# Kernel optimization log

Hardware: AMD Instinct MI355X
Metric: run time of the kernel (lower is better)

The kernel has to match this reference:

```python
import jax, jax.numpy as jnp
import numpy as np

B, N, D_POINTS, D_MODEL = 2, 2048, 32, 512


def _gather(feat, idx):
    # feat: [B, N, C], idx: [B, N, K] -> [B, N, K, C]
    return jax.vmap(lambda f, i: f[i])(feat, idx)


def setup_inputs() -> dict:
    key = jax.random.key(0)
    ks = jax.random.split(key, 20)
    def lin(k, fan_in, fan_out):
        bound = 1.0 / np.sqrt(fan_in)
        return jax.random.uniform(k, (fan_in, fan_out), jnp.float32, -bound, bound)
    def bias(k, fan_in, fan_out):
        bound = 1.0 / np.sqrt(fan_in)
        return jax.random.uniform(k, (fan_out,), jnp.float32, -bound, bound)
    return {
        "xyz": jax.random.normal(ks[0], (B, N, 3), jnp.float32),
        "points": jax.random.normal(ks[1], (B, N, D_POINTS), jnp.float32),
        "fc1_w": lin(ks[2], D_POINTS, D_MODEL), "fc1_b": bias(ks[3], D_POINTS, D_MODEL),
        "fc2_w": lin(ks[4], D_MODEL, D_POINTS), "fc2_b": bias(ks[5], D_MODEL, D_POINTS),
        "delta_w1": lin(ks[6], 3, D_MODEL), "delta_b1": bias(ks[7], 3, D_MODEL),
        "delta_w2": lin(ks[8], D_MODEL, D_MODEL), "delta_b2": bias(ks[9], D_MODEL, D_MODEL),
        "gamma_w1": lin(ks[10], D_MODEL, D_MODEL), "gamma_b1": bias(ks[11], D_MODEL, D_MODEL),
        "gamma_w2": lin(ks[12], D_MODEL, D_MODEL), "gamma_b2": bias(ks[13], D_MODEL, D_MODEL),
        "wq": lin(ks[14], D_MODEL, D_MODEL),
        "wk": lin(ks[15], D_MODEL, D_MODEL),
        "wv": lin(ks[16], D_MODEL, D_MODEL),
        "knn_k": 16,
    }


def reference(xyz, points, fc1_w, fc1_b, fc2_w, fc2_b,
              delta_w1, delta_b1, delta_w2, delta_b2,
              gamma_w1, gamma_b1, gamma_w2, gamma_b2,
              wq, wk, wv, knn_k):
    # square_distance: [B, N, N]
    sq = jnp.sum(xyz * xyz, axis=-1)
    dists = sq[:, :, None] + sq[:, None, :] - 2.0 * jnp.einsum('bnc,bmc->bnm', xyz, xyz)
    # knn: k smallest distances (argsort[:, :, :k] equivalent)
    _, knn_idx = jax.lax.top_k(-dists, knn_k)           # [B, N, K]
    knn_xyz = _gather(xyz, knn_idx)                      # [B, N, K, 3]

    pre = points
    x = points @ fc1_w + fc1_b                           # [B, N, d_model]
    q = x @ wq                                           # [B, N, d_model]
    k = _gather(x @ wk, knn_idx)                         # [B, N, K, d_model]
    v = _gather(x @ wv, knn_idx)                         # [B, N, K, d_model]

    # positional encoding MLP on delta xyz
    delta = xyz[:, :, None, :] - knn_xyz                 # [B, N, K, 3]
    pos_enc = jax.nn.relu(delta @ delta_w1 + delta_b1) @ delta_w2 + delta_b2

    # gamma MLP on (q - k + pos_enc)
    a = q[:, :, None, :] - k + pos_enc
    a = jax.nn.relu(a @ gamma_w1 + gamma_b1) @ gamma_w2 + gamma_b2

    scale = jnp.asarray(np.sqrt(D_MODEL), a.dtype)
    attn = jax.nn.softmax(a / scale, axis=-2)            # softmax over neighbors, per channel

    res = jnp.sum(attn * (v + pos_enc), axis=2)          # einsum 'bmnf,bmnf->bmf'
    res = res @ fc2_w + fc2_b + pre                      # [B, N, d_points]
    return res, attn
```

## Files before the change

kernel.cpp:

```cpp
#include <hip/hip_runtime.h>
#include <hip/hip_bf16.h>
#include <math.h>

typedef __bf16 bf16_t;
typedef float f32x4 __attribute__((ext_vector_type(4)));
typedef bf16_t bf16x8 __attribute__((ext_vector_type(8)));

#define BM 128
#define BN 128
#define BKT 32
#define NT 16

#define GLD_LDS16(gp, lp) __builtin_amdgcn_global_load_lds( \
    (const __attribute__((address_space(1))) void*)(gp), \
    (__attribute__((address_space(3))) void*)(lp), 16, 0, 0)

struct TC7 { const float* src[7]; bf16_t* dst[7]; };
__global__ __launch_bounds__(256) void tcast7_kernel(TC7 tc) {
  int job = blockIdx.x >> 10;
  int idx = (blockIdx.x & 1023) * 256 + threadIdx.x;
  if (job < 4) {
    int n = idx >> 9, k = idx & 511;
    tc.dst[job][idx] = (bf16_t)tc.src[job][k * 512 + n];
  } else {
    tc.dst[job][idx] = (bf16_t)tc.src[job][idx];
  }
}

__global__ __launch_bounds__(256) void cc_kernel(const float* __restrict__ db2, const float* __restrict__ gw1,
                                                 const float* __restrict__ gb1, float* __restrict__ cc) {
  int n = blockIdx.x * 256 + threadIdx.x;
  float s = gb1[n];
  for (int d = 0; d < 512; ++d) s = fmaf(db2[d], gw1[d * 512 + n], s);
  cc[n] = s;
}

__global__ __launch_bounds__(256) void knn_kernel(const float* __restrict__ xyz, int* __restrict__ knn) {
  __shared__ float sx[2048], sy[2048], sz[2048], sq[2048];
  int tid = threadIdx.x;
  int lane = tid & 63, wave = tid >> 6;
  int gq = blockIdx.x * 4 + wave;
  int b  = gq >> 11;
  int base = b << 11;
  for (int p = tid; p < 2048; p += 256) {
    float x = xyz[(base + p) * 3 + 0];
    float y = xyz[(base + p) * 3 + 1];
    float z = xyz[(base + p) * 3 + 2];
    sx[p] = x; sy[p] = y; sz[p] = z;
    sq[p] = __fadd_rn(__fadd_rn(__fmul_rn(x, x), __fmul_rn(y, y)), __fmul_rn(z, z));
  }
  __syncthreads();
  int iq = gq & 2047;
  float qx = sx[iq], qy = sy[iq], qz = sz[iq], sqi = sq[iq];

  unsigned long long key[32];
  #pragma unroll
  for (int j = 0; j < 32; ++j) {
    int p = lane + j * 64;
    float d = __fmul_rn(sx[p], qx);
    d = fmaf(sy[p], qy, d);
    d = fmaf(sz[p], qz, d);
    float dist = __fsub_rn(__fadd_rn(sqi, sq[p]), __fmul_rn(2.0f, d));
    unsigned int bits = __float_as_uint(dist);
    unsigned int sk = bits ^ (unsigned int)(((int)bits >> 31) | 0x80000000);
    key[j] = ((unsigned long long)sk << 32) | (unsigned int)p;
  }

  int r = 0;
  #pragma unroll 1
  for (int s = 0; s < 16; ++s) {
    unsigned long long m = key[0];
    #pragma unroll
    for (int j = 1; j < 32; ++j) m = (key[j] < m) ? key[j] : m;
    #pragma unroll
    for (int off = 32; off > 0; off >>= 1) {
      unsigned long long o = (unsigned long long)__shfl_xor((long long)m, off);
      if (o < m) m = o;
    }
    if (lane == s) r = base + (int)(m & 0xFFFFFFFFu);
    #pragma unroll
    for (int j = 0; j < 32; ++j) key[j] = (key[j] == m) ? ~0ULL : key[j];
  }
  if (lane < 16) knn[gq * 16 + lane] = r;
}

__global__ __launch_bounds__(256) void xfeat_kernel(const float* __restrict__ points, const float* __restrict__ fc1_w,
                                                    const float* __restrict__ fc1_b, bf16_t* __restrict__ xb) {
  __shared__ float p[32];
  int m = blockIdx.x, tid = threadIdx.x;
  if (tid < 32) p[tid] = points[m * 32 + tid];
  __syncthreads();
  for (int c = tid; c < 512; c += 256) {
    float a = fc1_b[c];
    #pragma unroll
    for (int kk = 0; kk < 32; ++kk) a = fmaf(p[kk], fc1_w[kk * 512 + c], a);
    xb[m * 512 + c] = (bf16_t)a;
  }
}

__global__ __launch_bounds__(256) void final_kernel(const float* __restrict__ res_mid, const float* __restrict__ fc2_w,
                                                    const float* __restrict__ fc2_b, const float* __restrict__ points,
                                                    float* __restrict__ out) {
  int oid = blockIdx.x * 256 + threadIdx.x;
  int m = oid >> 5, c = oid & 31;
  float a = fc2_b[c];
  const float* rm = res_mid + m * 512;
  for (int kk = 0; kk < 512; ++kk) a = fmaf(rm[kk], fc2_w[kk * 32 + c], a);
  out[oid] = a + points[oid];
}

struct GP {
  const bf16_t* A; const bf16_t* Bt; const bf16_t* Bt2;
  bf16_t* Cb; float* Cf; const float* bias; int ldc;
  const float* xyz; const int* knn; const float* dw1; const float* db1;
  const float* cc; const bf16_t* qkg;
  const bf16_t* vb; float* pe_attn; float* res_mid;
  const bf16_t* Aj[3]; bf16_t* Cbj[3];
};

template <int SRC, int EPI>
__global__ __launch_bounds__(256) void gemm_kernel(GP gp) {
  __shared__ bf16_t Alds[2 * BM * BKT];
  __shared__ bf16_t Blds[2 * BN * BKT];
  __shared__ bf16_t B2lds[(EPI == 5) ? (2 * BN * BKT) : 8];
  __shared__ float  wl[(SRC == 2) ? 4 * 512 : 8];
  int tid  = threadIdx.x;
  int lane = tid & 63, wave = tid >> 6;
  int wr = wave >> 1, wc = wave & 1;
  int lr = lane & 15, lg = lane >> 4;

  int gx = gridDim.x;
  int nwg = gx * gridDim.y;
  int orig = blockIdx.y * gx + blockIdx.x;
  int cpx = nwg >> 3;
  int swz = (orig & 7) * cpx + (orig >> 3);
  int bx = swz % gx;
  int by = swz / gx;
  int n0 = bx * BN;
  int m0 = ((EPI == 4) ? (by & 3) : by) * BM;
  const bf16_t* Aptr = (EPI == 4) ? gp.Aj[by >> 2] : gp.A;

  f32x4 acc[4][4];
  f32x4 acc2[(EPI == 5) ? 4 : 1][4];
  #pragma unroll
  for (int i = 0; i < 4; ++i)
    #pragma unroll
    for (int j = 0; j < 4; ++j) {
      acc[i][j] = (f32x4){0.f, 0.f, 0.f, 0.f};
      if (EPI == 5) acc2[i][j] = (f32x4){0.f, 0.f, 0.f, 0.f};
    }

  int rS2 = tid >> 2;
  int sl  = tid & 3;
  int swb = (rS2 >> 1) & 3;
  int scS = ((sl ^ swb) << 3);

  float dx0, dy0, dz0, dx1, dy1, dz1;
  if (SRC == 2) {
    for (int c = tid; c < 512; c += 256) {
      wl[c]        = gp.dw1[c];
      wl[512 + c]  = gp.dw1[512 + c];
      wl[1024 + c] = gp.dw1[1024 + c];
      wl[1536 + c] = gp.db1[c];
    }
    int m_a = m0 + rS2, m_b = m0 + rS2 + 64;
    int ga = m_a >> 4, ja = gp.knn[m_a];
    int gb = m_b >> 4, jb = gp.knn[m_b];
    dx0 = gp.xyz[ga * 3 + 0] - gp.xyz[ja * 3 + 0];
    dy0 = gp.xyz[ga * 3 + 1] - gp.xyz[ja * 3 + 1];
    dz0 = gp.xyz[ga * 3 + 2] - gp.xyz[ja * 3 + 2];
    dx1 = gp.xyz[gb * 3 + 0] - gp.xyz[jb * 3 + 0];
    dy1 = gp.xyz[gb * 3 + 1] - gp.xyz[jb * 3 + 1];
    dz1 = gp.xyz[gb * 3 + 2] - gp.xyz[jb * 3 + 2];
    __syncthreads();
  }

  auto stageA = [&](int t, int buf) {
    int k0 = t * BKT;
    if (SRC == 0) {
      GLD_LDS16(Aptr + (size_t)(m0 + rS2) * 512 + k0 + scS,       Alds + buf * (BM * BKT) + tid * 8);
      GLD_LDS16(Aptr + (size_t)(m0 + 64 + rS2) * 512 + k0 + scS,  Alds + buf * (BM * BKT) + 2048 + tid * 8);
    } else {
      int cb = k0 + sl * 8;
      f32x4 w0a = *(const f32x4*)(&wl[cb]),        w0b = *(const f32x4*)(&wl[cb + 4]);
      f32x4 w1a = *(const f32x4*)(&wl[512 + cb]),  w1b = *(const f32x4*)(&wl[512 + cb + 4]);
      f32x4 w2a = *(const f32x4*)(&wl[1024 + cb]), w2b = *(const f32x4*)(&wl[1024 + cb + 4]);
      f32x4 bba = *(const f32x4*)(&wl[1536 + cb]), bbb = *(const f32x4*)(&wl[1536 + cb + 4]);
      bf16_t* Ab = Alds + buf * (BM * BKT);
      bf16x8 o;
      #pragma unroll
      for (int u = 0; u < 4; ++u) {
        float h = fmaf(dz0, w2a[u], fmaf(dy0, w1a[u], dx0 * w0a[u])) + bba[u];
        o[u] = (bf16_t)fmaxf(h, 0.0f);
      }
      #pragma unroll
      for (int u = 0; u < 4; ++u) {
        float h = fmaf(dz0, w2b[u], fmaf(dy0, w1b[u], dx0 * w0b[u])) + bbb[u];
        o[4 + u] = (bf16_t)fmaxf(h, 0.0f);
      }
      *(bf16x8*)(&Ab[rS2 * BKT + ((sl ^ swb) << 3)]) = o;
      #pragma unroll
      for (int u = 0; u < 4; ++u) {
        float h = fmaf(dz1, w2a[u], fmaf(dy1, w1a[u], dx1 * w0a[u])) + bba[u];
        o[u] = (bf16_t)fmaxf(h, 0.0f);
      }
      #pragma unroll
      for (int u = 0; u < 4; ++u) {
        float h = fmaf(dz1, w2b[u], fmaf(dy1, w1b[u], dx1 * w0b[u])) + bbb[u];
        o[4 + u] = (bf16_t)fmaxf(h, 0.0f);
      }
      *(bf16x8*)(&Ab[(rS2 + 64) * BKT + ((sl ^ swb) << 3)]) = o;
    }
  };
  auto stageB = [&](int t, int buf) {
    int k0 = t * BKT;
    GLD_LDS16(gp.Bt + (size_t)(n0 + rS2) * 512 + k0 + scS,       Blds + buf * (BN * BKT) + tid * 8);
    GLD_LDS16(gp.Bt + (size_t)(n0 + 64 + rS2) * 512 + k0 + scS,  Blds + buf * (BN * BKT) + 2048 + tid * 8);
    if (EPI == 5) {
      GLD_LDS16(gp.Bt2 + (size_t)(n0 + rS2) * 512 + k0 + scS,      B2lds + buf * (BN * BKT) + tid * 8);
      GLD_LDS16(gp.Bt2 + (size_t)(n0 + 64 + rS2) * 512 + k0 + scS, B2lds + buf * (BN * BKT) + 2048 + tid * 8);
    }
  };
  auto mfmaPhase = [&](int cur) {
    const bf16_t* Ab = Alds + cur * (BM * BKT);
    const bf16_t* Bb = Blds + cur * (BN * BKT);
    const bf16_t* B2b = B2lds + cur * (BN * BKT);
    bf16x8 af[4], bfr[4], b2r[4];
    #pragma unroll
    for (int mi = 0; mi < 4; ++mi) {
      int rr = wr * 64 + mi * 16 + lr;
      af[mi] = *(const bf16x8*)(&Ab[rr * BKT + ((lg ^ ((rr >> 1) & 3)) << 3)]);
    }
    #pragma unroll
    for (int nj = 0; nj < 4; ++nj) {
      int rr = wc * 64 + nj * 16 + lr;
      bfr[nj] = *(const bf16x8*)(&Bb[rr * BKT + ((lg ^ ((rr >> 1) & 3)) << 3)]);
      if (EPI == 5) b2r[nj] = *(const bf16x8*)(&B2b[rr * BKT + ((lg ^ ((rr >> 1) & 3)) << 3)]);
    }
    #pragma unroll
    for (int mi = 0; mi < 4; ++mi)
      #pragma unroll
      for (int nj = 0; nj < 4; ++nj) {
        acc[mi][nj] = __builtin_amdgcn_mfma_f32_16x16x32_bf16(af[mi], bfr[nj], acc[mi][nj], 0, 0, 0);
        if (EPI == 5)
          acc2[mi][nj] = __builtin_amdgcn_mfma_f32_16x16x32_bf16(af[mi], b2r[nj], acc2[mi][nj], 0, 0, 0);
      }
  };

  stageA(0, 0);
  stageB(0, 0);

  #pragma unroll 1
  for (int t = 0; t < NT; ++t) {
    int cur = t & 1;
    if (SRC == 0) {
      if (t + 1 < NT) {
        stageA(t + 1, cur ^ 1);
        stageB(t + 1, cur ^ 1);
        asm volatile("s_waitcnt vmcnt(4)" ::: "memory");
      } else {
        asm volatile("s_waitcnt vmcnt(0)" ::: "memory");
      }
      __builtin_amdgcn_s_barrier();
      mfmaPhase(cur);
      __builtin_amdgcn_s_barrier();
    } else {
      if (t + 1 < NT) {
        stageB(t + 1, cur ^ 1);
        asm volatile("s_waitcnt vmcnt(4) lgkmcnt(0)" ::: "memory");
      } else {
        asm volatile("s_waitcnt vmcnt(0) lgkmcnt(0)" ::: "memory");
      }
      __builtin_amdgcn_s_barrier();
      __builtin_amdgcn_s_setprio(1);
      mfmaPhase(cur);
      __builtin_amdgcn_s_setprio(0);
      if (t + 1 < NT) stageA(t + 1, cur ^ 1);
      __builtin_amdgcn_s_barrier();
    }
  }

  if (EPI == 4) {
    bf16_t* CbT = gp.Cbj[by >> 2];
    #pragma unroll
    for (int mi = 0; mi < 4; ++mi)
      #pragma unroll
      for (int nj = 0; nj < 4; ++nj) {
        int col = n0 + wc * 64 + nj * 16 + lr;
        #pragma unroll
        for (int r = 0; r < 4; ++r) {
          int row = m0 + wr * 64 + mi * 16 + lg * 4 + r;
          CbT[(size_t)col * 512 + row] = (bf16_t)acc[mi][nj][r];
        }
      }
  } else if (EPI == 6) {
    #pragma unroll
    for (int mi = 0; mi < 4; ++mi)
      #pragma unroll
      for (int nj = 0; nj < 4; ++nj) {
        int col = n0 + wc * 64 + nj * 16 + lr;
        int part = col >> 9, c = col & 511;
        #pragma unroll
        for (int r = 0; r < 4; ++r) {
          int row = m0 + wr * 64 + mi * 16 + lg * 4 + r;
          gp.Cb[((size_t)part * 4096 + row) * 512 + c] = (bf16_t)acc[mi][nj][r];
        }
      }
  } else if (EPI == 5) {
    #pragma unroll
    for (int mi = 0; mi < 4; ++mi) {
      int g = (m0 + wr * 64 + mi * 16) >> 4;
      #pragma unroll
      for (int nj = 0; nj < 4; ++nj) {
        int col = n0 + wc * 64 + nj * 16 + lr;
        float db2v = gp.bias[col];
        float ccv  = gp.cc[col];
        float qgv  = (float)gp.qkg[((size_t)4096 + g) * 512 + col];
        #pragma unroll
        for (int r = 0; r < 4; ++r) {
          int row = m0 + wr * 64 + mi * 16 + lg * 4 + r;
          gp.Cf[(size_t)row * 512 + col] = acc[mi][nj][r] + db2v;
          int j = gp.knn[row];
          float kgv = (float)gp.qkg[((size_t)2 * 4096 + j) * 512 + col];
          float hv = acc2[mi][nj][r] + ccv + qgv - kgv;
          gp.Cb[(size_t)row * 512 + col] = (bf16_t)fmaxf(hv, 0.0f);
        }
      }
    }
  } else {
    const float scale = 22.62741699796952f;
    #pragma unroll
    for (int mi = 0; mi < 4; ++mi) {
      int g = (m0 + wr * 64 + mi * 16) >> 4;
      #pragma unroll
      for (int nj = 0; nj < 4; ++nj) {
        int col = n0 + wc * 64 + nj * 16 + lr;
        float sv[4];
        float mx = -INFINITY;
        #pragma unroll
        for (int r = 0; r < 4; ++r) {
          sv[r] = (acc[mi][nj][r] + gp.bias[col]) / scale;
          mx = fmaxf(mx, sv[r]);
        }
        mx = fmaxf(mx, __shfl_xor(mx, 16));
        mx = fmaxf(mx, __shfl_xor(mx, 32));
        float e[4], sum = 0.f;
        #pragma unroll
        for (int r = 0; r < 4; ++r) { e[r] = expf(sv[r] - mx); sum += e[r]; }
        sum += __shfl_xor(sum, 16);
        sum += __shfl_xor(sum, 32);
        float part = 0.f;
        #pragma unroll
        for (int r = 0; r < 4; ++r) {
          int row = g * 16 + lg * 4 + r;
          float at = e[r] / sum;
          int j = gp.knn[row];
          float vv  = (float)gp.vb[(size_t)j * 512 + col];
          float pev = gp.pe_attn[(size_t)row * 512 + col];
          part = fmaf(at, vv + pev, part);
          gp.pe_attn[(size_t)row * 512 + col] = at;
        }
        part += __shfl_xor(part, 16);
        part += __shfl_xor(part, 32);
        if (lg == 0) gp.res_mid[(size_t)g * 512 + col] = part;
      }
    }
  }
}

extern "C" void kernel_launch(void* const* d_in, const int* in_sizes, int n_in,
                              void* d_out, int out_size, void* d_ws, size_t ws_size,
                              hipStream_t stream) {
  const float* xyz    = (const float*)d_in[0];
  const float* points = (const float*)d_in[1];
  const float* fc1_w  = (const float*)d_in[2];
  const float* fc1_b  = (const float*)d_in[3];
  const float* fc2_w  = (const float*)d_in[4];
  const float* fc2_b  = (const float*)d_in[5];
  const float* dw1    = (const float*)d_in[6];
  const float* db1    = (const float*)d_in[7];
  const float* dw2    = (const float*)d_in[8];
  const float* db2    = (const float*)d_in[9];
  const float* gw1    = (const float*)d_in[10];
  const float* gb1    = (const float*)d_in[11];
  const float* gw2    = (const float*)d_in[12];
  const float* gb2    = (const float*)d_in[13];
  const float* wq     = (const float*)d_in[14];
  const float* wk     = (const float*)d_in[15];
  const float* wv     = (const float*)d_in[16];

  float* out = (float*)d_out;
  float* attn_pe = out + 131072;

  char* w = (char*)d_ws;
  bf16_t* wBig   = (bf16_t*)w; w += (size_t)1536 * 512 * 2;
  bf16_t* dw2T   = (bf16_t*)w; w += (size_t)512 * 512 * 2;
  bf16_t* gw1T   = (bf16_t*)w; w += (size_t)512 * 512 * 2;
  bf16_t* gw2T   = (bf16_t*)w; w += (size_t)512 * 512 * 2;
  bf16_t* dw2b   = (bf16_t*)w; w += (size_t)512 * 512 * 2;
  bf16_t* wqb    = (bf16_t*)w; w += (size_t)512 * 512 * 2;
  bf16_t* wkb    = (bf16_t*)w; w += (size_t)512 * 512 * 2;
  bf16_t* WpT    = (bf16_t*)w; w += (size_t)512 * 512 * 2;
  float*  cc     = (float*)w;  w += (size_t)512 * 4;
  int*    knn    = (int*)w;    w += (size_t)65536 * 4;
  bf16_t* xb     = (bf16_t*)w; w += (size_t)4096 * 512 * 2;
  bf16_t* vqkg   = (bf16_t*)w; w += (size_t)3 * 4096 * 512 * 2;
  bf16_t* h2     = (bf16_t*)w; w += (size_t)65536 * 512 * 2;
  float*  res_mid= (float*)w;  w += (size_t)4096 * 512 * 4;

  TC7 tc;
  tc.src[0] = wv;  tc.dst[0] = wBig;
  tc.src[1] = dw2; tc.dst[1] = dw2T;
  tc.src[2] = gw1; tc.dst[2] = gw1T;
  tc.src[3] = gw2; tc.dst[3] = gw2T;
  tc.src[4] = dw2; tc.dst[4] = dw2b;
  tc.src[5] = wq;  tc.dst[5] = wqb;
  tc.src[6] = wk;  tc.dst[6] = wkb;
  tcast7_kernel<<<7168, 256, 0, stream>>>(tc);

  knn_kernel<<<1024, 256, 0, stream>>>(xyz, knn);
  xfeat_kernel<<<4096, 256, 0, stream>>>(points, fc1_w, fc1_b, xb);
  cc_kernel<<<2, 256, 0, stream>>>(db2, gw1, gb1, cc);

  GP gwp{};
  gwp.Bt = gw1T;
  gwp.Aj[0] = dw2b; gwp.Cbj[0] = WpT;
  gwp.Aj[1] = wqb;  gwp.Cbj[1] = wBig + (size_t)512 * 512;
  gwp.Aj[2] = wkb;  gwp.Cbj[2] = wBig + (size_t)2 * 512 * 512;
  gemm_kernel<0, 4><<<dim3(4, 12), 256, 0, stream>>>(gwp);

  GP gq{};
  gq.A = xb; gq.Bt = wBig; gq.Cb = vqkg; gq.ldc = 1536;
  gemm_kernel<0, 6><<<dim3(12, 32), 256, 0, stream>>>(gq);

  GP gd{};
  gd.Bt = dw2T; gd.Bt2 = WpT; gd.Cf = attn_pe; gd.Cb = h2; gd.bias = db2;
  gd.xyz = xyz; gd.knn = knn; gd.dw1 = dw1; gd.db1 = db1;
  gd.cc = cc; gd.qkg = vqkg;
  gemm_kernel<2, 5><<<dim3(4, 512), 256, 0, stream>>>(gd);

  GP gs{};
  gs.A = h2; gs.Bt = gw2T; gs.bias = gb2;
  gs.knn = knn; gs.vb = vqkg; gs.pe_attn = attn_pe; gs.res_mid = res_mid;
  gemm_kernel<0, 3><<<dim3(4, 512), 256, 0, stream>>>(gs);

  final_kernel<<<512, 256, 0, stream>>>(res_mid, fc2_w, fc2_b, points, out);
}
```

Measured before the change: 501.2 us.

## Split dual-output positional GEMM into separate PE and gamma-input GEMMs

```diff
diff --git a/kernel.cpp b/kernel.cpp
--- a/kernel.cpp
+++ b/kernel.cpp
@@ -110,11 +110,11 @@
 }
 
 struct GP {
-  const bf16_t* A; const bf16_t* Bt; const bf16_t* Bt2;
-  bf16_t* Cb; float* Cf; const float* bias; int ldc;
+  const bf16_t* A; const bf16_t* Bt;
+  bf16_t* Cb; const float* bias; int ldc;
   const float* xyz; const int* knn; const float* dw1; const float* db1;
   const float* cc; const bf16_t* qkg;
-  const bf16_t* vb; float* pe_attn; float* res_mid;
+  const bf16_t* vb; const bf16_t* peb; float* attn; float* res_mid;
   const bf16_t* Aj[3]; bf16_t* Cbj[3];
 };
 
@@ -122,7 +122,6 @@
 __global__ __launch_bounds__(256) void gemm_kernel(GP gp) {
   __shared__ bf16_t Alds[2 * BM * BKT];
   __shared__ bf16_t Blds[2 * BN * BKT];
-  __shared__ bf16_t B2lds[(EPI == 5) ? (2 * BN * BKT) : 8];
   __shared__ float  wl[(SRC == 2) ? 4 * 512 : 8];
   int tid  = threadIdx.x;
   int lane = tid & 63, wave = tid >> 6;
@@ -141,14 +140,10 @@
   const bf16_t* Aptr = (EPI == 4) ? gp.Aj[by >> 2] : gp.A;
 
   f32x4 acc[4][4];
-  f32x4 acc2[(EPI == 5) ? 4 : 1][4];
   #pragma unroll
   for (int i = 0; i < 4; ++i)
     #pragma unroll
-    for (int j = 0; j < 4; ++j) {
-      acc[i][j] = (f32x4){0.f, 0.f, 0.f, 0.f};
-      if (EPI == 5) acc2[i][j] = (f32x4){0.f, 0.f, 0.f, 0.f};
-    }
+    for (int j = 0; j < 4; ++j) acc[i][j] = (f32x4){0.f, 0.f, 0.f, 0.f};
 
   int rS2 = tid >> 2;
   int sl  = tid & 3;
@@ -198,7 +193,7 @@
         float h = fmaf(dz0, w2b[u], fmaf(dy0, w1b[u], dx0 * w0b[u])) + bbb[u];
         o[4 + u] = (bf16_t)fmaxf(h, 0.0f);
       }
-      *(bf16x8*)(&Ab[rS2 * BKT + ((sl ^ swb) << 3)]) = o;
+      *(bf16x8*)(&Ab[rS2 * BKT + (scS ^ 0)]) = o;
       #pragma unroll
       for (int u = 0; u < 4; ++u) {
         float h = fmaf(dz1, w2a[u], fmaf(dy1, w1a[u], dx1 * w0a[u])) + bba[u];
@@ -209,23 +204,18 @@
         float h = fmaf(dz1, w2b[u], fmaf(dy1, w1b[u], dx1 * w0b[u])) + bbb[u];
         o[4 + u] = (bf16_t)fmaxf(h, 0.0f);
       }
-      *(bf16x8*)(&Ab[(rS2 + 64) * BKT + ((sl ^ swb) << 3)]) = o;
+      *(bf16x8*)(&Ab[(rS2 + 64) * BKT + (scS ^ 0)]) = o;
     }
   };
   auto stageB = [&](int t, int buf) {
     int k0 = t * BKT;
     GLD_LDS16(gp.Bt + (size_t)(n0 + rS2) * 512 + k0 + scS,       Blds + buf * (BN * BKT) + tid * 8);
     GLD_LDS16(gp.Bt + (size_t)(n0 + 64 + rS2) * 512 + k0 + scS,  Blds + buf * (BN * BKT) + 2048 + tid * 8);
-    if (EPI == 5) {
-      GLD_LDS16(gp.Bt2 + (size_t)(n0 + rS2) * 512 + k0 + scS,      B2lds + buf * (BN * BKT) + tid * 8);
-      GLD_LDS16(gp.Bt2 + (size_t)(n0 + 64 + rS2) * 512 + k0 + scS, B2lds + buf * (BN * BKT) + 2048 + tid * 8);
-    }
   };
   auto mfmaPhase = [&](int cur) {
     const bf16_t* Ab = Alds + cur * (BM * BKT);
     const bf16_t* Bb = Blds + cur * (BN * BKT);
-    const bf16_t* B2b = B2lds + cur * (BN * BKT);
-    bf16x8 af[4], bfr[4], b2r[4];
+    bf16x8 af[4], bfr[4];
     #pragma unroll
     for (int mi = 0; mi < 4; ++mi) {
       int rr = wr * 64 + mi * 16 + lr;
@@ -235,16 +225,12 @@
     for (int nj = 0; nj < 4; ++nj) {
       int rr = wc * 64 + nj * 16 + lr;
       bfr[nj] = *(const bf16x8*)(&Bb[rr * BKT + ((lg ^ ((rr >> 1) & 3)) << 3)]);
-      if (EPI == 5) b2r[nj] = *(const bf16x8*)(&B2b[rr * BKT + ((lg ^ ((rr >> 1) & 3)) << 3)]);
     }
     #pragma unroll
     for (int mi = 0; mi < 4; ++mi)
       #pragma unroll
-      for (int nj = 0; nj < 4; ++nj) {
+      for (int nj = 0; nj < 4; ++nj)
         acc[mi][nj] = __builtin_amdgcn_mfma_f32_16x16x32_bf16(af[mi], bfr[nj], acc[mi][nj], 0, 0, 0);
-        if (EPI == 5)
-          acc2[mi][nj] = __builtin_amdgcn_mfma_f32_16x16x32_bf16(af[mi], b2r[nj], acc2[mi][nj], 0, 0, 0);
-      }
   };
 
   stageA(0, 0);
@@ -253,31 +239,17 @@
   #pragma unroll 1
   for (int t = 0; t < NT; ++t) {
     int cur = t & 1;
-    if (SRC == 0) {
-      if (t + 1 < NT) {
-        stageA(t + 1, cur ^ 1);
-        stageB(t + 1, cur ^ 1);
-        asm volatile("s_waitcnt vmcnt(4)" ::: "memory");
-      } else {
-        asm volatile("s_waitcnt vmcnt(0)" ::: "memory");
-      }
-      __builtin_amdgcn_s_barrier();
-      mfmaPhase(cur);
-      __builtin_amdgcn_s_barrier();
+    if (t + 1 < NT) {
+      stageA(t + 1, cur ^ 1);
+      stageB(t + 1, cur ^ 1);
+      if (SRC == 0) asm volatile("s_waitcnt vmcnt(4)" ::: "memory");
+      else          asm volatile("s_waitcnt vmcnt(2) lgkmcnt(0)" ::: "memory");
     } else {
-      if (t + 1 < NT) {
-        stageB(t + 1, cur ^ 1);
-        asm volatile("s_waitcnt vmcnt(4) lgkmcnt(0)" ::: "memory");
-      } else {
-        asm volatile("s_waitcnt vmcnt(0) lgkmcnt(0)" ::: "memory");
-      }
-      __builtin_amdgcn_s_barrier();
-      __builtin_amdgcn_s_setprio(1);
-      mfmaPhase(cur);
-      __builtin_amdgcn_s_setprio(0);
-      if (t + 1 < NT) stageA(t + 1, cur ^ 1);
-      __builtin_amdgcn_s_barrier();
-    }
+      asm volatile("s_waitcnt vmcnt(0) lgkmcnt(0)" ::: "memory");
+    }
+    __builtin_amdgcn_s_barrier();
+    mfmaPhase(cur);
+    __builtin_amdgcn_s_barrier();
   }
 
   if (EPI == 4) {
@@ -306,23 +278,34 @@
           gp.Cb[((size_t)part * 4096 + row) * 512 + c] = (bf16_t)acc[mi][nj][r];
         }
       }
-  } else if (EPI == 5) {
+  } else if (EPI == 1) {
+    #pragma unroll
+    for (int mi = 0; mi < 4; ++mi)
+      #pragma unroll
+      for (int nj = 0; nj < 4; ++nj) {
+        int col = n0 + wc * 64 + nj * 16 + lr;
+        float bv = gp.bias[col];
+        #pragma unroll
+        for (int r = 0; r < 4; ++r) {
+          int row = m0 + wr * 64 + mi * 16 + lg * 4 + r;
+          gp.Cb[(size_t)row * 512 + col] = (bf16_t)(acc[mi][nj][r] + bv);
+        }
+      }
+  } else if (EPI == 2) {
     #pragma unroll
     for (int mi = 0; mi < 4; ++mi) {
       int g = (m0 + wr * 64 + mi * 16) >> 4;
       #pragma unroll
       for (int nj = 0; nj < 4; ++nj) {
         int col = n0 + wc * 64 + nj * 16 + lr;
-        float db2v = gp.bias[col];
-        float ccv  = gp.cc[col];
-        float qgv  = (float)gp.qkg[((size_t)4096 + g) * 512 + col];
+        float ccv = gp.cc[col];
+        float qgv = (float)gp.qkg[((size_t)4096 + g) * 512 + col];
         #pragma unroll
         for (int r = 0; r < 4; ++r) {
           int row = m0 + wr * 64 + mi * 16 + lg * 4 + r;
-          gp.Cf[(size_t)row * 512 + col] = acc[mi][nj][r] + db2v;
           int j = gp.knn[row];
           float kgv = (float)gp.qkg[((size_t)2 * 4096 + j) * 512 + col];
-          float hv = acc2[mi][nj][r] + ccv + qgv - kgv;
+          float hv = acc[mi][nj][r] + ccv + qgv - kgv;
           gp.Cb[(size_t)row * 512 + col] = (bf16_t)fmaxf(hv, 0.0f);
         }
       }
@@ -356,9 +339,9 @@
           float at = e[r] / sum;
           int j = gp.knn[row];
           float vv  = (float)gp.vb[(size_t)j * 512 + col];
-          float pev = gp.pe_attn[(size_t)row * 512 + col];
+          float pev = (float)gp.peb[(size_t)row * 512 + col];
           part = fmaf(at, vv + pev, part);
-          gp.pe_attn[(size_t)row * 512 + col] = at;
+          gp.attn[(size_t)row * 512 + col] = at;
         }
         part += __shfl_xor(part, 16);
         part += __shfl_xor(part, 32);
@@ -390,7 +373,7 @@
   const float* wv     = (const float*)d_in[16];
 
   float* out = (float*)d_out;
-  float* attn_pe = out + 131072;
+  float* attn = out + 131072;
 
   char* w = (char*)d_ws;
   bf16_t* wBig   = (bf16_t*)w; w += (size_t)1536 * 512 * 2;
@@ -405,6 +388,7 @@
   int*    knn    = (int*)w;    w += (size_t)65536 * 4;
   bf16_t* xb     = (bf16_t*)w; w += (size_t)4096 * 512 * 2;
   bf16_t* vqkg   = (bf16_t*)w; w += (size_t)3 * 4096 * 512 * 2;
+  bf16_t* peb    = (bf16_t*)w; w += (size_t)65536 * 512 * 2;
   bf16_t* h2     = (bf16_t*)w; w += (size_t)65536 * 512 * 2;
   float*  res_mid= (float*)w;  w += (size_t)4096 * 512 * 4;
 
@@ -433,15 +417,20 @@
   gq.A = xb; gq.Bt = wBig; gq.Cb = vqkg; gq.ldc = 1536;
   gemm_kernel<0, 6><<<dim3(12, 32), 256, 0, stream>>>(gq);
 
-  GP gd{};
-  gd.Bt = dw2T; gd.Bt2 = WpT; gd.Cf = attn_pe; gd.Cb = h2; gd.bias = db2;
-  gd.xyz = xyz; gd.knn = knn; gd.dw1 = dw1; gd.db1 = db1;
-  gd.cc = cc; gd.qkg = vqkg;
-  gemm_kernel<2, 5><<<dim3(4, 512), 256, 0, stream>>>(gd);
+  GP gpe{};
+  gpe.Bt = dw2T; gpe.Cb = peb; gpe.bias = db2;
+  gpe.xyz = xyz; gpe.knn = knn; gpe.dw1 = dw1; gpe.db1 = db1;
+  gemm_kernel<2, 1><<<dim3(4, 512), 256, 0, stream>>>(gpe);
+
+  GP gg{};
+  gg.Bt = WpT; gg.Cb = h2;
+  gg.xyz = xyz; gg.knn = knn; gg.dw1 = dw1; gg.db1 = db1;
+  gg.cc = cc; gg.qkg = vqkg;
+  gemm_kernel<2, 2><<<dim3(4, 512), 256, 0, stream>>>(gg);
 
   GP gs{};
   gs.A = h2; gs.Bt = gw2T; gs.bias = gb2;
-  gs.knn = knn; gs.vb = vqkg; gs.pe_attn = attn_pe; gs.res_mid = res_mid;
+  gs.knn = knn; gs.vb = vqkg; gs.peb = peb; gs.attn = attn; gs.res_mid = res_mid;
   gemm_kernel<0, 3><<<dim3(4, 512), 256, 0, stream>>>(gs);
 
   final_kernel<<<512, 256, 0, stream>>>(res_mid, fc2_w, fc2_b, points, out);
```

Result: faster. 436.7 us (-12.9%).
